# Optimization experiments

Hardware: AMD Instinct MI355X
Metric: run time of the kernel (lower is better)

The kernel has to match this reference:

```python
import jax, jax.numpy as jnp
import numpy as np

B, S, D, H = 4, 1024, 1024, 16
DH = D // H  # per-head dim


def setup_inputs() -> dict:
    key = jax.random.key(0)
    ks = jax.random.split(key, 9)
    f = lambda k, sh: jax.random.normal(k, sh, dtype=jnp.float32)
    return {
        "query": f(ks[0], (B, S, D)),
        "key": f(ks[1], (B, S, D)),
        "value": f(ks[2], (B, S, D)),
        "mask": jax.random.randint(ks[3], (B, S), 0, 2).astype(jnp.int32),
        "pos_emb": f(ks[4], (H, S, DH)),
        "W_q": f(ks[5], (D, D)) * 0.02,
        "W_k": f(ks[6], (D, D)) * 0.02,
        "W_v": f(ks[7], (D, D)) * 0.02,
        "W_o": f(ks[8], (D, D)) * 0.02,
    }


def _shift(x):
    """Music-Transformer skew trick. x: [b,h,i,j] -> [b,h,i,j]."""
    b, h, i, j = x.shape
    x = jnp.concatenate([x, jnp.zeros((b, h, i, i), x.dtype)], axis=-1)  # [b,h,i,i+j]
    l = i + j - 1
    flat = x.reshape(b, h, i * (i + j))
    pad = (-flat.shape[-1]) % l
    flat = jnp.concatenate([flat, jnp.zeros((b, h, pad), flat.dtype)], axis=-1)
    return flat.reshape(b, h, -1, l)[:, :, :i, i - 1:]


def reference(query, key, value, mask, pos_emb, W_q, W_k, W_v, W_o):
    b, s, _ = query.shape
    # torch Linear(bias=False): y = x @ W.T ; then split heads -> [b,h,s,dh]
    proj = lambda x, W: (x @ W.T).reshape(b, s, H, DH).transpose(0, 2, 1, 3)
    q = proj(query, W_q)
    k = proj(key, W_k)
    v = proj(value, W_v)

    dots = jnp.einsum('bhid,bhjd->bhij', q, k) * (DH ** -0.5)
    pe = pos_emb[:, :s, :]  # [h,s,dh]
    # NOTE: original code scales positional scores by dim ** (+0.5)
    pos_dots = jnp.einsum('bhid,hjd->bhij', q, pe) * (DH ** 0.5)
    dots = dots + _shift(pos_dots)

    m = (mask[:, :, None] * mask[:, None, :])[:, None]  # [b,1,s,s]
    dots = jnp.where(m == 0, jnp.float32(-1e9), dots)

    attn = jax.nn.softmax(dots, axis=-1)  # dropout omitted (eval / p=0)
    x = jnp.einsum('bhij,bhjd->bhid', attn, v)
    x = x.transpose(0, 2, 1, 3).reshape(b, s, H * DH)
    return x @ W_o.T
```

## Files before the change

### kernel.cpp

```cpp
#include <hip/hip_runtime.h>
#include <math.h>

#define BB 4
#define SS 1024
#define DD 1024
#define HH 16
#define DHH 64

typedef _Float16 half8 __attribute__((ext_vector_type(8)));
typedef _Float16 half4v __attribute__((ext_vector_type(4)));
typedef float v4f __attribute__((ext_vector_type(4)));
typedef unsigned int u32;
typedef unsigned short u16;

__device__ __forceinline__ void gload_lds16(const void* g, void* l) {
    __builtin_amdgcn_global_load_lds(
        (const __attribute__((address_space(1))) u32*)(const u32*)g,
        (__attribute__((address_space(3))) u32*)(u32*)l, 16, 0, 0);
}

__global__ __launch_bounds__(256) void convert_kernel(
    const float* __restrict__ wq, const float* __restrict__ wk,
    const float* __restrict__ wv, const float* __restrict__ wo,
    const float* __restrict__ pe, _Float16* __restrict__ dst)
{
    const int i4 = blockIdx.x * 256 + threadIdx.x;
    const int region = i4 >> 18;
    const int local4 = i4 & 262143;
    const float* srcs[5] = {wq, wk, wv, wo, pe};
    const float scales[5] = {1.0f, 0.125f, 1.0f, 1.0f, 8.0f};
    const float sc = scales[region];
    float4 v = *(const float4*)(srcs[region] + (size_t)local4 * 4);
    half4v h = {(_Float16)(v.x * sc), (_Float16)(v.y * sc),
                (_Float16)(v.z * sc), (_Float16)(v.w * sc)};
    *(half4v*)(dst + ((size_t)region << 20) + (size_t)local4 * 4) = h;
}

__global__ __launch_bounds__(256) void convert2_kernel(
    const float* __restrict__ wq, const float* __restrict__ wk,
    const float* __restrict__ wv, const float* __restrict__ wo,
    const float* __restrict__ pe, const float* __restrict__ q,
    const float* __restrict__ k, const float* __restrict__ vv,
    _Float16* __restrict__ dst)
{
    const int i4 = blockIdx.x * 256 + threadIdx.x;
    const int region = i4 >> 18;
    const int local4 = i4 & 262143;
    const float* src;
    float sc = 1.0f;
    if (region == 0)      { src = wq; }
    else if (region == 1) { src = wk; sc = 0.125f; }
    else if (region == 2) { src = wv; }
    else if (region == 3) { src = wo; }
    else if (region == 4) { src = pe; sc = 8.0f; }
    else if (region < 9)  { src = q  + ((size_t)(region - 5)  << 20); }
    else if (region < 13) { src = k  + ((size_t)(region - 9)  << 20); }
    else                  { src = vv + ((size_t)(region - 13) << 20); }
    float4 v = *(const float4*)(src + (size_t)local4 * 4);
    half4v h = {(_Float16)(v.x * sc), (_Float16)(v.y * sc),
                (_Float16)(v.z * sc), (_Float16)(v.w * sc)};
    *(half4v*)(dst + ((size_t)region << 20) + (size_t)local4 * 4) = h;
}

__global__ __launch_bounds__(256) void gemm_proj_f32(
    const float* __restrict__ Aq, const float* __restrict__ Ak,
    const float* __restrict__ Av,
    const _Float16* __restrict__ Wqf, const _Float16* __restrict__ Wkf,
    const _Float16* __restrict__ Wvf,
    _Float16* __restrict__ Cq, _Float16* __restrict__ Ck,
    _Float16* __restrict__ Cv)
{
    __shared__ _Float16 As[128 * 32];
    __shared__ _Float16 Bs[64 * 32];

    const int z = blockIdx.z;
    const float* A = z == 0 ? Aq : z == 1 ? Ak : Av;
    const _Float16* W = z == 0 ? Wqf : z == 1 ? Wkf : Wvf;
    _Float16* C = z == 0 ? Cq : z == 1 ? Ck : Cv;

    const int tid = threadIdx.x;
    const int w = tid >> 6, lane = tid & 63, lm = lane & 15, quad = lane >> 4;
    const int n0 = blockIdx.x * 64, m0 = blockIdx.y * 128;

    const int brow = tid >> 2, blc = (tid & 3) ^ (brow & 3);

    v4f zero4 = {0.f, 0.f, 0.f, 0.f};
    v4f acc[2][4];
#pragma unroll
    for (int mi = 0; mi < 2; mi++)
#pragma unroll
        for (int ni = 0; ni < 4; ni++) acc[mi][ni] = zero4;

    for (int k0 = 0; k0 < DD; k0 += 32) {
        __syncthreads();
        gload_lds16(W + (size_t)(n0 + brow) * DD + k0 + blc * 8, Bs + tid * 8);
#pragma unroll
        for (int u = 0; u < 4; u++) {
            int c4 = tid + 256 * u;
            int row = c4 >> 3, k4 = c4 & 7;
            float4 v = *(const float4*)(A + (size_t)(m0 + row) * DD + k0 + k4 * 4);
            half4v hv = {(_Float16)v.x, (_Float16)v.y, (_Float16)v.z, (_Float16)v.w};
            int c16 = k4 >> 1, hlf = k4 & 1;
            *(half4v*)(As + row * 32 + (((c16 ^ (row & 3)) << 3) + (hlf << 2))) = hv;
        }
        __syncthreads();

        half8 af[2], bf[4];
#pragma unroll
        for (int mi = 0; mi < 2; mi++) {
            int row = w * 32 + mi * 16 + lm;
            af[mi] = *(const half8*)(As + row * 32 + ((quad ^ (row & 3)) << 3));
        }
#pragma unroll
        for (int ni = 0; ni < 4; ni++) {
            int row = ni * 16 + lm;
            bf[ni] = *(const half8*)(Bs + row * 32 + ((quad ^ (row & 3)) << 3));
        }
#pragma unroll
        for (int mi = 0; mi < 2; mi++)
#pragma unroll
            for (int ni = 0; ni < 4; ni++)
                acc[mi][ni] = __builtin_amdgcn_mfma_f32_16x16x32_f16(
                    af[mi], bf[ni], acc[mi][ni], 0, 0, 0);
    }

    const int h = n0 >> 6;
#pragma unroll
    for (int mi = 0; mi < 2; mi++)
#pragma unroll
        for (int r = 0; r < 4; r++) {
            int m = m0 + w * 32 + mi * 16 + quad * 4 + r;
            int b = m >> 10, s = m & 1023;
            size_t base = ((size_t)(b * HH + h) * SS + s) * DHH;
#pragma unroll
            for (int ni = 0; ni < 4; ni++)
                C[base + ni * 16 + lm] = (_Float16)acc[mi][ni][r];
        }
}

__global__ __launch_bounds__(256) void gemm_proj_f16_128(
    const _Float16* __restrict__ Aq, const _Float16* __restrict__ Ak,
    const _Float16* __restrict__ Av,
    const _Float16* __restrict__ Wqf, const _Float16* __restrict__ Wkf,
    const _Float16* __restrict__ Wvf,
    _Float16* __restrict__ Cq, _Float16* __restrict__ Ck,
    _Float16* __restrict__ Cv)
{
    __shared__ _Float16 As[2][128 * 32];
    __shared__ _Float16 Bs[2][128 * 32];

    const int z = blockIdx.z;
    const _Float16* A = z == 0 ? Aq : z == 1 ? Ak : Av;
    const _Float16* W = z == 0 ? Wqf : z == 1 ? Wkf : Wvf;
    _Float16* C = z == 0 ? Cq : z == 1 ? Ck : Cv;

    const int tid = threadIdx.x;
    const int w = tid >> 6, lane = tid & 63, lm = lane & 15, quad = lane >> 4;
    const int wr = (w >> 1) * 64, wc = (w & 1) * 64;
    const int n0 = blockIdx.x * 128, m0 = blockIdx.y * 128;

    const int srow0 = tid >> 2,          slc0 = (tid & 3) ^ (srow0 & 3);
    const int srow1 = (tid + 256) >> 2,  slc1 = ((tid + 256) & 3) ^ (srow1 & 3);

    v4f zero4 = {0.f, 0.f, 0.f, 0.f};
    v4f acc[4][4];
#pragma unroll
    for (int mi = 0; mi < 4; mi++)
#pragma unroll
        for (int ni = 0; ni < 4; ni++) acc[mi][ni] = zero4;

    gload_lds16(W + (size_t)(n0 + srow0) * DD + slc0 * 8, &Bs[0][tid * 8]);
    gload_lds16(A + (size_t)(m0 + srow0) * DD + slc0 * 8, &As[0][tid * 8]);
    gload_lds16(W + (size_t)(n0 + srow1) * DD + slc1 * 8, &Bs[0][(tid + 256) * 8]);
    gload_lds16(A + (size_t)(m0 + srow1) * DD + slc1 * 8, &As[0][(tid + 256) * 8]);
    __syncthreads();

    for (int kt = 0; kt < 32; kt++) {
        const int cur = kt & 1;
        if (kt + 1 < 32) {
            const int k0n = (kt + 1) * 32;
            gload_lds16(W + (size_t)(n0 + srow0) * DD + k0n + slc0 * 8, &Bs[cur ^ 1][tid * 8]);
            gload_lds16(A + (size_t)(m0 + srow0) * DD + k0n + slc0 * 8, &As[cur ^ 1][tid * 8]);
            gload_lds16(W + (size_t)(n0 + srow1) * DD + k0n + slc1 * 8, &Bs[cur ^ 1][(tid + 256) * 8]);
            gload_lds16(A + (size_t)(m0 + srow1) * DD + k0n + slc1 * 8, &As[cur ^ 1][(tid + 256) * 8]);
        }

        half8 af[4], bf[4];
#pragma unroll
        for (int mi = 0; mi < 4; mi++) {
            int row = wr + mi * 16 + lm;
            af[mi] = *(const half8*)(&As[cur][0] + row * 32 + ((quad ^ (row & 3)) << 3));
        }
#pragma unroll
        for (int ni = 0; ni < 4; ni++) {
            int row = wc + ni * 16 + lm;
            bf[ni] = *(const half8*)(&Bs[cur][0] + row * 32 + ((quad ^ (row & 3)) << 3));
        }
        __builtin_amdgcn_s_setprio(1);
#pragma unroll
        for (int mi = 0; mi < 4; mi++)
#pragma unroll
            for (int ni = 0; ni < 4; ni++)
                acc[mi][ni] = __builtin_amdgcn_mfma_f32_16x16x32_f16(
                    af[mi], bf[ni], acc[mi][ni], 0, 0, 0);
        __builtin_amdgcn_s_setprio(0);

        __syncthreads();
    }

#pragma unroll
    for (int mi = 0; mi < 4; mi++)
#pragma unroll
        for (int r = 0; r < 4; r++) {
            int m = m0 + wr + mi * 16 + quad * 4 + r;
            int b = m >> 10, s = m & 1023;
#pragma unroll
            for (int ni = 0; ni < 4; ni++) {
                int n = n0 + wc + ni * 16 + lm;
                int h = n >> 6, d = n & 63;
                C[((size_t)(b * HH + h) * SS + s) * DHH + d] = (_Float16)acc[mi][ni][r];
            }
        }
}

__global__ __launch_bounds__(256) void gemm_out_128(
    const _Float16* __restrict__ A, const _Float16* __restrict__ W,
    float* __restrict__ C)
{
    __shared__ _Float16 As[2][128 * 32];
    __shared__ _Float16 Bs[2][128 * 32];

    const int tid = threadIdx.x;
    const int w = tid >> 6, lane = tid & 63, lm = lane & 15, quad = lane >> 4;
    const int wr = (w >> 1) * 64, wc = (w & 1) * 64;
    const int n0 = blockIdx.x * 128, m0 = blockIdx.y * 128;

    const int srow0 = tid >> 2,          slc0 = (tid & 3) ^ (srow0 & 3);
    const int srow1 = (tid + 256) >> 2,  slc1 = ((tid + 256) & 3) ^ (srow1 & 3);

    v4f zero4 = {0.f, 0.f, 0.f, 0.f};
    v4f acc[4][4];
#pragma unroll
    for (int mi = 0; mi < 4; mi++)
#pragma unroll
        for (int ni = 0; ni < 4; ni++) acc[mi][ni] = zero4;

    gload_lds16(W + (size_t)(n0 + srow0) * DD + slc0 * 8, &Bs[0][tid * 8]);
    gload_lds16(A + (size_t)(m0 + srow0) * DD + slc0 * 8, &As[0][tid * 8]);
    gload_lds16(W + (size_t)(n0 + srow1) * DD + slc1 * 8, &Bs[0][(tid + 256) * 8]);
    gload_lds16(A + (size_t)(m0 + srow1) * DD + slc1 * 8, &As[0][(tid + 256) * 8]);
    __syncthreads();

    for (int kt = 0; kt < 32; kt++) {
        const int cur = kt & 1;
        if (kt + 1 < 32) {
            const int k0n = (kt + 1) * 32;
            gload_lds16(W + (size_t)(n0 + srow0) * DD + k0n + slc0 * 8, &Bs[cur ^ 1][tid * 8]);
            gload_lds16(A + (size_t)(m0 + srow0) * DD + k0n + slc0 * 8, &As[cur ^ 1][tid * 8]);
            gload_lds16(W + (size_t)(n0 + srow1) * DD + k0n + slc1 * 8, &Bs[cur ^ 1][(tid + 256) * 8]);
            gload_lds16(A + (size_t)(m0 + srow1) * DD + k0n + slc1 * 8, &As[cur ^ 1][(tid + 256) * 8]);
        }

        half8 af[4], bf[4];
#pragma unroll
        for (int mi = 0; mi < 4; mi++) {
            int row = wr + mi * 16 + lm;
            af[mi] = *(const half8*)(&As[cur][0] + row * 32 + ((quad ^ (row & 3)) << 3));
        }
#pragma unroll
        for (int ni = 0; ni < 4; ni++) {
            int row = wc + ni * 16 + lm;
            bf[ni] = *(const half8*)(&Bs[cur][0] + row * 32 + ((quad ^ (row & 3)) << 3));
        }
        __builtin_amdgcn_s_setprio(1);
#pragma unroll
        for (int mi = 0; mi < 4; mi++)
#pragma unroll
            for (int ni = 0; ni < 4; ni++)
                acc[mi][ni] = __builtin_amdgcn_mfma_f32_16x16x32_f16(
                    af[mi], bf[ni], acc[mi][ni], 0, 0, 0);
        __builtin_amdgcn_s_setprio(0);

        __syncthreads();
    }

#pragma unroll
    for (int mi = 0; mi < 4; mi++)
#pragma unroll
        for (int r = 0; r < 4; r++) {
            size_t base = (size_t)(m0 + wr + mi * 16 + quad * 4 + r) * DD
                        + n0 + wc + lm;
#pragma unroll
            for (int ni = 0; ni < 4; ni++)
                C[base + ni * 16] = acc[mi][ni][r];
        }
}

__global__ __launch_bounds__(256) void gemm_out(
    const _Float16* __restrict__ A, const _Float16* __restrict__ W,
    float* __restrict__ C)
{
    __shared__ _Float16 As[128 * 32];
    __shared__ _Float16 Bs[64 * 32];

    const int tid = threadIdx.x;
    const int w = tid >> 6, lane = tid & 63, lm = lane & 15, quad = lane >> 4;
    const int n0 = blockIdx.x * 64, m0 = blockIdx.y * 128;
    const int brow = tid >> 2, blc = (tid & 3) ^ (brow & 3);

    v4f zero4 = {0.f, 0.f, 0.f, 0.f};
    v4f acc[2][4];
#pragma unroll
    for (int mi = 0; mi < 2; mi++)
#pragma unroll
        for (int ni = 0; ni < 4; ni++) acc[mi][ni] = zero4;

    for (int k0 = 0; k0 < DD; k0 += 32) {
        __syncthreads();
        gload_lds16(W + (size_t)(n0 + brow) * DD + k0 + blc * 8, Bs + tid * 8);
#pragma unroll
        for (int u = 0; u < 2; u++) {
            int p = tid + 256 * u;
            int row = p >> 2, lc = (p & 3) ^ (row & 3);
            gload_lds16(A + (size_t)(m0 + row) * DD + k0 + lc * 8, As + p * 8);
        }
        __syncthreads();

        half8 af[2], bf[4];
#pragma unroll
    for (int mi = 0; mi < 2; mi++) {
            int row = w * 32 + mi * 16 + lm;
            af[mi] = *(const half8*)(As + row * 32 + ((quad ^ (row & 3)) << 3));
        }
#pragma unroll
        for (int ni = 0; ni < 4; ni++) {
            int row = ni * 16 + lm;
            bf[ni] = *(const half8*)(Bs + row * 32 + ((quad ^ (row & 3)) << 3));
        }
#pragma unroll
        for (int mi = 0; mi < 2; mi++)
#pragma unroll
            for (int ni = 0; ni < 4; ni++)
                acc[mi][ni] = __builtin_amdgcn_mfma_f32_16x16x32_f16(
                    af[mi], bf[ni], acc[mi][ni], 0, 0, 0);
    }

#pragma unroll
    for (int mi = 0; mi < 2; mi++)
#pragma unroll
        for (int r = 0; r < 4; r++) {
            size_t base = (size_t)(m0 + w * 32 + mi * 16 + quad * 4 + r) * DD
                        + n0 + lm;
#pragma unroll
            for (int ni = 0; ni < 4; ni++)
                C[base + ni * 16] = acc[mi][ni][r];
        }
}

__global__ __launch_bounds__(256) void attn_mfma(
    const _Float16* __restrict__ Qg, const _Float16* __restrict__ Kg,
    const _Float16* __restrict__ Vg, const int* __restrict__ mask,
    const _Float16* __restrict__ peg, _Float16* __restrict__ Og)
{
    __shared__ _Float16 Ks[64 * 64];
    __shared__ _Float16 Vt[64 * 64];
    __shared__ _Float16 PEb[128 * 64];
    __shared__ _Float16 Pb[4][16 * 64];

    const int tid = threadIdx.x;
    const int w = tid >> 6, lane = tid & 63;
    const int lm = lane & 15, quad = lane >> 4;

    const int lid = blockIdx.y * 16 + blockIdx.x;
    const int it = ((lid & 15) + ((lid >> 8) << 2)) & 15;
    const int bh = lid >> 4;
    const int i0 = it * 64;
    const int b = bh >> 4, h = bh & 15;

    const _Float16* Qb = Qg + (size_t)bh * SS * DHH;
    const _Float16* Kb = Kg + (size_t)bh * SS * DHH;
    const _Float16* Vb = Vg + (size_t)bh * SS * DHH;
    const _Float16* peh = peg + (size_t)h * SS * DHH;

    float mi_f[4];
#pragma unroll
    for (int r = 0; r < 4; r++)
        mi_f[r] = (float)mask[b * SS + i0 + w * 16 + quad * 4 + r];

    half8 qf[2];
#pragma unroll
    for (int kc = 0; kc < 2; kc++)
        qf[kc] = *(const half8*)(Qb + (size_t)(i0 + w * 16 + lm) * DHH
                                 + kc * 32 + quad * 8);

    const int srow = tid >> 3, sk8 = tid & 7;
    const int lmx = (lm & 7) << 3;

    half8 ones8 = {(_Float16)1, (_Float16)1, (_Float16)1, (_Float16)1,
                   (_Float16)1, (_Float16)1, (_Float16)1, (_Float16)1};

    v4f zero4 = {0.f, 0.f, 0.f, 0.f};
    float m_run[4];
    v4f oacc[4], lacc;
#pragma unroll
    for (int r = 0; r < 4; r++) m_run[r] = -1e30f;
#pragma unroll
    for (int nb = 0; nb < 4; nb++) oacc[nb] = zero4;
    lacc = zero4;

    half8 kreg[2], vreg[2], pereg[4];
#pragma unroll
    for (int u = 0; u < 2; u++) {
        int row = srow + 32 * u;
        kreg[u] = *(const half8*)(Kb + (size_t)row * DHH + sk8 * 8);
        vreg[u] = *(const half8*)(Vb + (size_t)row * DHH + sk8 * 8);
    }
    {
        const int g0 = SS - 1 - i0 - 63;
#pragma unroll
        for (int u = 0; u < 4; u++) {
            int o = srow + 32 * u;
            int g = g0 + o;
            half8 v = {0, 0, 0, 0, 0, 0, 0, 0};
            if (g < SS) v = *(const half8*)(peh + (size_t)g * DHH + sk8 * 8);
            pereg[u] = v;
        }
    }

    for (int jt = 0; jt < SS / 64; jt++) {
        const int j0 = jt * 64;
        const bool do_pe = (jt <= it);
        __syncthreads();

#pragma unroll
        for (int u = 0; u < 2; u++) {
            int row = srow + 32 * u;
            *(half8*)(Ks + row * 64 + ((sk8 * 8) ^ ((row & 7) << 3))) = kreg[u];
        }
#pragma unroll
        for (int u = 0; u < 2; u++) {
            int row = srow + 32 * u;
            int jsw = row ^ (sk8 << 3);
#pragma unroll
            for (int e = 0; e < 8; e++) Vt[(sk8 * 8 + e) * 64 + jsw] = vreg[u][e];
        }
        if (do_pe) {
#pragma unroll
            for (int u = 0; u < 4; u++) {
                int o = srow + 32 * u;
                *(half8*)(PEb + o * 64 + ((sk8 * 8) ^ ((o & 7) << 3))) = pereg[u];
            }
        }
        float mj_f[4];
#pragma unroll
        for (int nb = 0; nb < 4; nb++)
            mj_f[nb] = (float)mask[b * SS + j0 + nb * 16 + lm];
        __syncthreads();

        if (jt + 1 < SS / 64) {
            const int j0n = j0 + 64;
#pragma unroll
            for (int u = 0; u < 2; u++) {
                int row = srow + 32 * u;
                kreg[u] = *(const half8*)(Kb + (size_t)(j0n + row) * DHH + sk8 * 8);
                vreg[u] = *(const half8*)(Vb + (size_t)(j0n + row) * DHH + sk8 * 8);
            }
            if (jt + 1 <= it) {
                const int g0n = SS - 1 + j0n - i0 - 63;
#pragma unroll
                for (int u = 0; u < 4; u++) {
                    int o = srow + 32 * u;
                    int g = g0n + o;
                    half8 v = {0, 0, 0, 0, 0, 0, 0, 0};
                    if (g < SS) v = *(const half8*)(peh + (size_t)g * DHH + sk8 * 8);
                    pereg[u] = v;
                }
            }
        }

        v4f sacc[4];
#pragma unroll
        for (int nb = 0; nb < 4; nb++) sacc[nb] = zero4;
        __builtin_amdgcn_s_setprio(1);
#pragma unroll
        for (int nb = 0; nb < 4; nb++)
#pragma unroll
            for (int kc = 0; kc < 2; kc++) {
                half8 kf = *(const half8*)(Ks + (nb * 16 + lm) * 64
                                           + ((kc * 32 + quad * 8) ^ lmx));
                sacc[nb] = __builtin_amdgcn_mfma_f32_16x16x32_f16(qf[kc], kf, sacc[nb], 0, 0, 0);
            }
        __builtin_amdgcn_s_setprio(0);

        if (do_pe) {
            v4f racc[5];
#pragma unroll
            for (int e = 0; e < 5; e++) racc[e] = zero4;
            __builtin_amdgcn_s_setprio(1);
#pragma unroll
            for (int e = 0; e < 5; e++) {
                int row = (e + 3 - w) * 16 + lm;
#pragma unroll
                for (int kc = 0; kc < 2; kc++) {
                    half8 pf = *(const half8*)(PEb + row * 64
                                               + ((kc * 32 + quad * 8) ^ lmx));
                    racc[e] = __builtin_amdgcn_mfma_f32_16x16x32_f16(qf[kc], pf, racc[e], 0, 0, 0);
                }
            }
            __builtin_amdgcn_s_setprio(0);
#pragma unroll
            for (int nb = 0; nb < 4; nb++)
#pragma unroll
                for (int r = 0; r < 4; r++) {
                    int qr = quad * 4 + r;
                    float vsrc = (((lm + qr + 1) & 15) <= qr)
                               ? racc[nb][r] : racc[nb + 1][r];
                    int src = (lane & 48) | ((lm - qr - 1) & 15);
                    sacc[nb][r] += __shfl(vsrc, src);
                }
        }

        float p[4][4];
        float alpha[4];
#pragma unroll
        for (int i = 0; i < 4; i++) {
            float mi = mi_f[i];
            float rmax = -1e30f;
#pragma unroll
            for (int j = 0; j < 4; j++) {
                float s = sacc[j][i];
                if (mi * mj_f[j] == 0.f) s = -1e9f;
                sacc[j][i] = s;
                rmax = fmaxf(rmax, s);
            }
#pragma unroll
            for (int off = 1; off < 16; off <<= 1)
                rmax = fmaxf(rmax, __shfl_xor(rmax, off));
            float mnew = fmaxf(m_run[i], rmax);
            alpha[i] = __expf(m_run[i] - mnew);
            m_run[i] = mnew;
#pragma unroll
            for (int j = 0; j < 4; j++)
                p[j][i] = __expf(sacc[j][i] - mnew);
        }

        _Float16* Pw = &Pb[w][0];
#pragma unroll
        for (int nb = 0; nb < 4; nb++)
#pragma unroll
            for (int r = 0; r < 4; r++) {
                int qr = quad * 4 + r;
                Pw[qr * 64 + ((nb * 16 + lm) ^ ((qr & 7) << 3))] = (_Float16)p[nb][r];
            }
#pragma unroll
        for (int nb = 0; nb < 4; nb++)
#pragma unroll
            for (int r = 0; r < 4; r++) oacc[nb][r] *= alpha[r];
#pragma unroll
        for (int r = 0; r < 4; r++) lacc[r] *= alpha[r];

        __builtin_amdgcn_s_setprio(1);
#pragma unroll
        for (int kc = 0; kc < 2; kc++) {
            half8 pfrag = *(const half8*)(Pw + lm * 64 + ((kc * 32 + quad * 8) ^ lmx));
            lacc = __builtin_amdgcn_mfma_f32_16x16x32_f16(pfrag, ones8, lacc, 0, 0, 0);
#pragma unroll
            for (int nb = 0; nb < 4; nb++) {
                int d = nb * 16 + lm;
                int col = (kc * 32 + quad * 8) ^ (((d >> 3) & 7) << 3);
                half8 vfrag = *(const half8*)(Vt + d * 64 + col);
                oacc[nb] = __builtin_amdgcn_mfma_f32_16x16x32_f16(pfrag, vfrag, oacc[nb], 0, 0, 0);
            }
        }
        __builtin_amdgcn_s_setprio(0);
    }

#pragma unroll
    for (int r = 0; r < 4; r++) {
        float inv = 1.f / lacc[r];
        int s = i0 + w * 16 + quad * 4 + r;
#pragma unroll
        for (int nb = 0; nb < 4; nb++)
            Og[((size_t)b * SS + s) * DD + h * DHH + nb * 16 + lm] =
                (_Float16)(oacc[nb][r] * inv);
    }
}

extern "C" void kernel_launch(void* const* d_in, const int* in_sizes, int n_in,
                              void* d_out, int out_size, void* d_ws, size_t ws_size,
                              hipStream_t stream)
{
    const float* query = (const float*)d_in[0];
    const float* key   = (const float*)d_in[1];
    const float* value = (const float*)d_in[2];
    const int*   mask  = (const int*)d_in[3];
    const float* pe    = (const float*)d_in[4];
    const float* Wq    = (const float*)d_in[5];
    const float* Wk    = (const float*)d_in[6];
    const float* Wv    = (const float*)d_in[7];
    const float* Wo    = (const float*)d_in[8];
    float* out = (float*)d_out;

    _Float16* ws16 = (_Float16*)d_ws;
    const size_t MEG = 1048576;
    _Float16* wqf = ws16;
    _Float16* wkf = ws16 + 1 * MEG;
    _Float16* wvf = ws16 + 2 * MEG;
    _Float16* wof = ws16 + 3 * MEG;
    _Float16* pef = ws16 + 4 * MEG;

    const bool big = ws_size >= (size_t)33 * MEG * sizeof(_Float16);

    if (big) {
        _Float16* q16 = ws16 + 5 * MEG;
        _Float16* k16 = ws16 + 9 * MEG;
        _Float16* v16 = ws16 + 13 * MEG;
        _Float16* qp  = ws16 + 17 * MEG;
        _Float16* kp  = ws16 + 21 * MEG;
        _Float16* vp  = ws16 + 25 * MEG;
        _Float16* ao  = ws16 + 29 * MEG;

        convert2_kernel<<<17408, 256, 0, stream>>>(
            Wq, Wk, Wv, Wo, pe, query, key, value, ws16);

        gemm_proj_f16_128<<<dim3(DD / 128, (BB * SS) / 128, 3), 256, 0, stream>>>(
            q16, k16, v16, wqf, wkf, wvf, qp, kp, vp);

        attn_mfma<<<dim3(SS / 64, BB * HH), 256, 0, stream>>>(
            qp, kp, vp, mask, pef, ao);

        gemm_out_128<<<dim3(DD / 128, (BB * SS) / 128), 256, 0, stream>>>(ao, wof, out);
    } else {
        _Float16* qp  = ws16 + 5 * MEG;
        _Float16* kp  = ws16 + 9 * MEG;
        _Float16* vp  = ws16 + 13 * MEG;
        _Float16* ao  = ws16 + 17 * MEG;

        convert_kernel<<<5120, 256, 0, stream>>>(Wq, Wk, Wv, Wo, pe, ws16);

        gemm_proj_f32<<<dim3(DD / 64, (BB * SS) / 128, 3), 256, 0, stream>>>(
            query, key, value, wqf, wkf, wvf, qp, kp, vp);

        attn_mfma<<<dim3(SS / 64, BB * HH), 256, 0, stream>>>(
            qp, kp, vp, mask, pef, ao);

        gemm_out<<<dim3(DD / 64, (BB * SS) / 128), 256, 0, stream>>>(ao, wof, out);
    }
}
```

Baseline: 275.3 us.

## Triple-buffer LDS in projection and output GEMMs with partial vmcnt waits

Replaces the double-buffered global-to-LDS pipeline in the QKV projection and output GEMMs with a three-stage ring. Loads are issued two K-tiles ahead, and the loop waits with s_waitcnt vmcnt(4) plus one barrier per iteration instead of a full __syncthreads. This keeps one tile's loads in flight during compute, to hide global memory latency. It raises LDS use from 32KB to 48KB per block, which can lower occupancy, and correctness depends on the hand-counted vmcnt.

```diff
diff --git a/kernel.cpp b/kernel.cpp
--- a/kernel.cpp
+++ b/kernel.cpp
@@ -146,8 +146,8 @@
     _Float16* __restrict__ Cq, _Float16* __restrict__ Ck,
     _Float16* __restrict__ Cv)
 {
-    __shared__ _Float16 As[2][128 * 32];
-    __shared__ _Float16 Bs[2][128 * 32];
+    __shared__ _Float16 As[3][128 * 32];
+    __shared__ _Float16 Bs[3][128 * 32];
 
     const int z = blockIdx.z;
     const _Float16* A = z == 0 ? Aq : z == 1 ? Ak : Av;
@@ -169,32 +169,39 @@
 #pragma unroll
         for (int ni = 0; ni < 4; ni++) acc[mi][ni] = zero4;
 
-    gload_lds16(W + (size_t)(n0 + srow0) * DD + slc0 * 8, &Bs[0][tid * 8]);
-    gload_lds16(A + (size_t)(m0 + srow0) * DD + slc0 * 8, &As[0][tid * 8]);
-    gload_lds16(W + (size_t)(n0 + srow1) * DD + slc1 * 8, &Bs[0][(tid + 256) * 8]);
-    gload_lds16(A + (size_t)(m0 + srow1) * DD + slc1 * 8, &As[0][(tid + 256) * 8]);
-    __syncthreads();
+#define STAGE_PROJ(KT, BUF) do {                                              \
+        const int _k0 = (KT) * 32;                                            \
+        gload_lds16(W + (size_t)(n0 + srow0) * DD + _k0 + slc0 * 8,           \
+                    &Bs[BUF][tid * 8]);                                       \
+        gload_lds16(A + (size_t)(m0 + srow0) * DD + _k0 + slc0 * 8,           \
+                    &As[BUF][tid * 8]);                                       \
+        gload_lds16(W + (size_t)(n0 + srow1) * DD + _k0 + slc1 * 8,           \
+                    &Bs[BUF][(tid + 256) * 8]);                               \
+        gload_lds16(A + (size_t)(m0 + srow1) * DD + _k0 + slc1 * 8,           \
+                    &As[BUF][(tid + 256) * 8]);                               \
+    } while (0)
+
+    STAGE_PROJ(0, 0);
+    STAGE_PROJ(1, 1);
 
     for (int kt = 0; kt < 32; kt++) {
-        const int cur = kt & 1;
-        if (kt + 1 < 32) {
-            const int k0n = (kt + 1) * 32;
-            gload_lds16(W + (size_t)(n0 + srow0) * DD + k0n + slc0 * 8, &Bs[cur ^ 1][tid * 8]);
-            gload_lds16(A + (size_t)(m0 + srow0) * DD + k0n + slc0 * 8, &As[cur ^ 1][tid * 8]);
-            gload_lds16(W + (size_t)(n0 + srow1) * DD + k0n + slc1 * 8, &Bs[cur ^ 1][(tid + 256) * 8]);
-            gload_lds16(A + (size_t)(m0 + srow1) * DD + k0n + slc1 * 8, &As[cur ^ 1][(tid + 256) * 8]);
-        }
-
+        if (kt < 31) asm volatile("s_waitcnt vmcnt(4)" ::: "memory");
+        else         asm volatile("s_waitcnt vmcnt(0)" ::: "memory");
+        __builtin_amdgcn_s_barrier();
+        if (kt + 2 < 32) STAGE_PROJ(kt + 2, (kt + 2) % 3);
+
+        const _Float16* Ab = &As[kt % 3][0];
+        const _Float16* Bb = &Bs[kt % 3][0];
         half8 af[4], bf[4];
 #pragma unroll
         for (int mi = 0; mi < 4; mi++) {
             int row = wr + mi * 16 + lm;
-            af[mi] = *(const half8*)(&As[cur][0] + row * 32 + ((quad ^ (row & 3)) << 3));
+            af[mi] = *(const half8*)(Ab + row * 32 + ((quad ^ (row & 3)) << 3));
         }
 #pragma unroll
         for (int ni = 0; ni < 4; ni++) {
             int row = wc + ni * 16 + lm;
-            bf[ni] = *(const half8*)(&Bs[cur][0] + row * 32 + ((quad ^ (row & 3)) << 3));
+            bf[ni] = *(const half8*)(Bb + row * 32 + ((quad ^ (row & 3)) << 3));
         }
         __builtin_amdgcn_s_setprio(1);
 #pragma unroll
@@ -204,9 +211,8 @@
                 acc[mi][ni] = __builtin_amdgcn_mfma_f32_16x16x32_f16(
                     af[mi], bf[ni], acc[mi][ni], 0, 0, 0);
         __builtin_amdgcn_s_setprio(0);
-
-        __syncthreads();
-    }
+    }
+#undef STAGE_PROJ
 
 #pragma unroll
     for (int mi = 0; mi < 4; mi++)
@@ -227,8 +233,8 @@
     const _Float16* __restrict__ A, const _Float16* __restrict__ W,
     float* __restrict__ C)
 {
-    __shared__ _Float16 As[2][128 * 32];
-    __shared__ _Float16 Bs[2][128 * 32];
+    __shared__ _Float16 As[3][128 * 32];
+    __shared__ _Float16 Bs[3][128 * 32];
 
     const int tid = threadIdx.x;
     const int w = tid >> 6, lane = tid & 63, lm = lane & 15, quad = lane >> 4;
@@ -245,32 +251,39 @@
 #pragma unroll
         for (int ni = 0; ni < 4; ni++) acc[mi][ni] = zero4;
 
-    gload_lds16(W + (size_t)(n0 + srow0) * DD + slc0 * 8, &Bs[0][tid * 8]);
-    gload_lds16(A + (size_t)(m0 + srow0) * DD + slc0 * 8, &As[0][tid * 8]);
-    gload_lds16(W + (size_t)(n0 + srow1) * DD + slc1 * 8, &Bs[0][(tid + 256) * 8]);
-    gload_lds16(A + (size_t)(m0 + srow1) * DD + slc1 * 8, &As[0][(tid + 256) * 8]);
-    __syncthreads();
+#define STAGE_OUT(KT, BUF) do {                                               \
+        const int _k0 = (KT) * 32;                                            \
+        gload_lds16(W + (size_t)(n0 + srow0) * DD + _k0 + slc0 * 8,           \
+                    &Bs[BUF][tid * 8]);                                       \
+        gload_lds16(A + (size_t)(m0 + srow0) * DD + _k0 + slc0 * 8,           \
+                    &As[BUF][tid * 8]);                                       \
+        gload_lds16(W + (size_t)(n0 + srow1) * DD + _k0 + slc1 * 8,           \
+                    &Bs[BUF][(tid + 256) * 8]);                               \
+        gload_lds16(A + (size_t)(m0 + srow1) * DD + _k0 + slc1 * 8,           \
+                    &As[BUF][(tid + 256) * 8]);                               \
+    } while (0)
+
+    STAGE_OUT(0, 0);
+    STAGE_OUT(1, 1);
 
     for (int kt = 0; kt < 32; kt++) {
-        const int cur = kt & 1;
-        if (kt + 1 < 32) {
-            const int k0n = (kt + 1) * 32;
-            gload_lds16(W + (size_t)(n0 + srow0) * DD + k0n + slc0 * 8, &Bs[cur ^ 1][tid * 8]);
-            gload_lds16(A + (size_t)(m0 + srow0) * DD + k0n + slc0 * 8, &As[cur ^ 1][tid * 8]);
-            gload_lds16(W + (size_t)(n0 + srow1) * DD + k0n + slc1 * 8, &Bs[cur ^ 1][(tid + 256) * 8]);
-            gload_lds16(A + (size_t)(m0 + srow1) * DD + k0n + slc1 * 8, &As[cur ^ 1][(tid + 256) * 8]);
-        }
-
+        if (kt < 31) asm volatile("s_waitcnt vmcnt(4)" ::: "memory");
+        else         asm volatile("s_waitcnt vmcnt(0)" ::: "memory");
+        __builtin_amdgcn_s_barrier();
+        if (kt + 2 < 32) STAGE_OUT(kt + 2, (kt + 2) % 3);
+
+        const _Float16* Ab = &As[kt % 3][0];
+        const _Float16* Bb = &Bs[kt % 3][0];
         half8 af[4], bf[4];
 #pragma unroll
         for (int mi = 0; mi < 4; mi++) {
             int row = wr + mi * 16 + lm;
-            af[mi] = *(const half8*)(&As[cur][0] + row * 32 + ((quad ^ (row & 3)) << 3));
+            af[mi] = *(const half8*)(Ab + row * 32 + ((quad ^ (row & 3)) << 3));
         }
 #pragma unroll
         for (int ni = 0; ni < 4; ni++) {
             int row = wc + ni * 16 + lm;
-            bf[ni] = *(const half8*)(&Bs[cur][0] + row * 32 + ((quad ^ (row & 3)) << 3));
+            bf[ni] = *(const half8*)(Bb + row * 32 + ((quad ^ (row & 3)) << 3));
         }
         __builtin_amdgcn_s_setprio(1);
 #pragma unroll
@@ -280,9 +293,8 @@
                 acc[mi][ni] = __builtin_amdgcn_mfma_f32_16x16x32_f16(
                     af[mi], bf[ni], acc[mi][ni], 0, 0, 0);
         __builtin_amdgcn_s_setprio(0);
-
-        __syncthreads();
-    }
+    }
+#undef STAGE_OUT
 
 #pragma unroll
     for (int mi = 0; mi < 4; mi++)
```

Result: no change. 275.1 us (-0.1%).
